# Performance work log

Measured on AMD Instinct MI355X. Metric: run time of the kernel, lower is better.

The kernel has to match this reference:

```python
import jax, jax.numpy as jnp
import numpy as np

P = 32
EPS = 1e-5

def setup_inputs() -> dict:
    key = jax.random.key(0)
    ks = jax.random.split(key, 6)
    B, C, H, W = 2, 256, 512, 512
    h_past = jax.random.normal(ks[0], (B, C, H, W), dtype=jnp.float32)
    scale = jnp.ones((C,), jnp.float32)
    shift = jnp.zeros((C,), jnp.float32)
    # depthwise 3x3: torch Conv2d(ch, ch, 3, groups=ch) weight shape (C,1,3,3)
    dw_w = jax.random.normal(ks[1], (C, 1, 3, 3), dtype=jnp.float32) * (1.0 / 3.0)
    dw_b = jax.random.normal(ks[2], (C,), dtype=jnp.float32) * 0.02
    # pointwise 1x1: weight (C_out, C_in)
    pw_w = jax.random.normal(ks[3], (C, C), dtype=jnp.float32) * (1.0 / np.sqrt(C))
    pw_b = jax.random.normal(ks[4], (C,), dtype=jnp.float32) * 0.02
    return {"h_past": h_past, "scale": scale, "shift": shift,
            "dw_w": dw_w, "dw_b": dw_b, "pw_w": pw_w, "pw_b": pw_b}

def reference(h_past, scale, shift, dw_w, dw_b, pw_w, pw_b):
    B, C, H, W = h_past.shape
    NRp, NCp = H // P, W // P
    # block-mean pool: [B,C,NRp,P,NCp,P] -> [B,C,NRp,NCp]
    x = h_past.reshape(B, C, NRp, P, NCp, P).mean(axis=(3, 5))
    # channel norm (mean/var over channel dim, unbiased=False)
    mu = x.mean(axis=1, keepdims=True)
    var = x.var(axis=1, keepdims=True)
    x = (x - mu) * jax.lax.rsqrt(var + EPS)
    x = x * scale[None, :, None, None] + shift[None, :, None, None]
    # depthwise 3x3 conv, padding=1
    x = jax.lax.conv_general_dilated(
        x, dw_w, window_strides=(1, 1), padding=((1, 1), (1, 1)),
        feature_group_count=C,
        dimension_numbers=("NCHW", "OIHW", "NCHW"))
    x = x + dw_b[None, :, None, None]
    # exact GELU (torch F.gelu default)
    x = jax.nn.gelu(x, approximate=False)
    # pointwise 1x1 conv
    x = jnp.einsum("bchw,oc->bohw", x, pw_w) + pw_b[None, :, None, None]
    # broadcast-upsample back to full H x W
    x_full = jnp.broadcast_to(x[:, :, :, None, :, None], (B, C, NRp, P, NCp, P))
    return x_full.reshape(B, C, NRp * P, NCp * P)
```

## Files before the change

kernel.cpp:

```cpp
#include <hip/hip_runtime.h>
#include <math.h>

constexpr int B = 2, C = 256, H = 512, W = 512, P = 32;
constexpr int NR = H / P;
constexpr int NC = W / P;
constexpr int NPOS = NR * NC;
constexpr float EPS = 1e-5f;

typedef float floatx4 __attribute__((ext_vector_type(4)));

__global__ void pool_kernel(const float* __restrict__ h_past,
                            float* __restrict__ xp) {
    int bid = blockIdx.x;
    int br = bid & 15;
    int c  = (bid >> 4) & 255;
    int b  = bid >> 12;
    const floatx4* src =
        (const floatx4*)(h_past + (((size_t)(b * C + c)) * H + (size_t)br * P) * W);
    int t    = threadIdx.x;
    int f4   = t & 127;
    int row0 = t >> 7;
    float s = 0.f;
#pragma unroll
    for (int k = 0; k < 16; ++k) {
        floatx4 v = src[(row0 + 2 * k) * 128 + f4];
        s += v.x + v.y + v.z + v.w;
    }
    __shared__ float part[256];
    part[t] = s;
    __syncthreads();
    if (t < 16) {
        float acc = 0.f;
#pragma unroll
        for (int j = 0; j < 8; ++j)
            acc += part[t * 8 + j] + part[128 + t * 8 + j];
        xp[((size_t)(b * NPOS + br * NC + t)) * C + c] = acc * (1.0f / (P * P));
    }
}

__global__ void stats_kernel(const float* __restrict__ xp,
                             float* __restrict__ mu_arr,
                             float* __restrict__ rs_arr) {
    int bid = blockIdx.x;
    int t = threadIdx.x;
    float v = xp[(size_t)bid * C + t];
    __shared__ float red[8];
    float s = v;
#pragma unroll
    for (int off = 32; off > 0; off >>= 1) s += __shfl_down(s, off, 64);
    int wave = t >> 6, lane = t & 63;
    if (lane == 0) red[wave] = s;
    __syncthreads();
    float mu = (red[0] + red[1] + red[2] + red[3]) * (1.0f / C);
    float d = v - mu;
    float s2 = d * d;
#pragma unroll
    for (int off = 32; off > 0; off >>= 1) s2 += __shfl_down(s2, off, 64);
    if (lane == 0) red[4 + wave] = s2;
    __syncthreads();
    if (t == 0) {
        float var = (red[4] + red[5] + red[6] + red[7]) * (1.0f / C);
        mu_arr[bid] = mu;
        rs_arr[bid] = rsqrtf(var + EPS);
    }
}

__global__ void pwt_kernel(const float* __restrict__ pw_w,
                           floatx4* __restrict__ pw_t) {
    int idx = blockIdx.x * 256 + threadIdx.x;
    int c4 = idx >> 8;
    int o  = idx & 255;
    const float* src = pw_w + o * C + 4 * c4;
    floatx4 v = {src[0], src[1], src[2], src[3]};
    pw_t[idx] = v;
}

__device__ inline float gelu_exact(float x) {
    return 0.5f * x * (1.0f + erff(x * 0.70710678118654752440f));
}

__global__ void fused_kernel(const float* __restrict__ xp,
                             const float* __restrict__ mu_arr,
                             const float* __restrict__ rs_arr,
                             const float* __restrict__ scale,
                             const float* __restrict__ shift,
                             const float* __restrict__ dw_w,
                             const float* __restrict__ dw_b,
                             const floatx4* __restrict__ pw_t,
                             const float* __restrict__ pw_b,
                             float* __restrict__ z) {
    int bid = blockIdx.x;
    int p = bid & 255;
    int b = bid >> 8;
    int h = p >> 4;
    int w = p & 15;
    int c = threadIdx.x;

    float sc = scale[c];
    float sh = shift[c];
    const float* wt  = dw_w + c * 9;
    const float* xpb = xp + (size_t)b * NPOS * C;
    const float* mub = mu_arr + b * NPOS;
    const float* rsb = rs_arr + b * NPOS;

    float acc = 0.f;
#pragma unroll
    for (int kh = 0; kh < 3; ++kh) {
        int hh = h + kh - 1;
        if (hh < 0 || hh >= NR) continue;
#pragma unroll
        for (int kw = 0; kw < 3; ++kw) {
            int ww = w + kw - 1;
            if (ww < 0 || ww >= NC) continue;
            int q = hh * NC + ww;
            float xv = xpb[(size_t)q * C + c];
            float xn = (xv - mub[q]) * rsb[q] * sc + sh;
            acc += xn * wt[kh * 3 + kw];
        }
    }
    float yv = gelu_exact(acc + dw_b[c]);

    __shared__ float ys[256];
    ys[c] = yv;
    __syncthreads();

    const floatx4* yv4 = (const floatx4*)ys;
    float acc2 = 0.f;
#pragma unroll 4
    for (int c4 = 0; c4 < 64; ++c4) {
        floatx4 wv = pw_t[c4 * 256 + c];
        floatx4 vv = yv4[c4];
        acc2 += wv.x * vv.x + wv.y * vv.y + wv.z * vv.z + wv.w * vv.w;
    }
    z[(size_t)bid * C + c] = acc2 + pw_b[c];
}

__global__ void up_kernel(const float* __restrict__ z,
                          floatx4* __restrict__ out) {
    const int total = B * C * H * (W / 4);
    for (int idx = blockIdx.x * 256 + threadIdx.x; idx < total;
         idx += gridDim.x * 256) {
        int w4 = idx & 127;
        int h  = (idx >> 7) & 511;
        int bc = idx >> 16;
        int b  = bc >> 8;
        int c  = bc & 255;
        int p  = (h >> 5) * NC + (w4 >> 3);
        float v = z[((size_t)(b * NPOS + p)) * C + c];
        floatx4 o = {v, v, v, v};
        out[idx] = o;
    }
}

extern "C" void kernel_launch(void* const* d_in, const int* in_sizes, int n_in,
                              void* d_out, int out_size, void* d_ws, size_t ws_size,
                              hipStream_t stream) {
    const float* h_past = (const float*)d_in[0];
    const float* scale  = (const float*)d_in[1];
    const float* shift  = (const float*)d_in[2];
    const float* dw_w   = (const float*)d_in[3];
    const float* dw_b   = (const float*)d_in[4];
    const float* pw_w   = (const float*)d_in[5];
    const float* pw_b   = (const float*)d_in[6];
    float* out = (float*)d_out;

    float* ws = (float*)d_ws;
    const int SMALL = B * C * NPOS;
    float* xp   = ws;
    float* z    = ws + SMALL;
    float* mu   = ws + 2 * SMALL;
    float* rs   = mu + B * NPOS;
    floatx4* pw_t = (floatx4*)(rs + B * NPOS);

    pwt_kernel<<<64, 256, 0, stream>>>(pw_w, pw_t);
    pool_kernel<<<B * C * NR, 256, 0, stream>>>(h_past, xp);
    stats_kernel<<<B * NPOS, 256, 0, stream>>>(xp, mu, rs);
    fused_kernel<<<B * NPOS, 256, 0, stream>>>(xp, mu, rs, scale, shift,
                                               dw_w, dw_b, pw_t, pw_b, z);
    up_kernel<<<32768, 256, 0, stream>>>(z, (floatx4*)out);
}
```

Before: 895.7 us.

## Merge all stages into one cooperative kernel with grid-wide syncs

```diff
diff --git a/kernel.cpp b/kernel.cpp
--- a/kernel.cpp
+++ b/kernel.cpp
@@ -1,5 +1,8 @@
 #include <hip/hip_runtime.h>
+#include <hip/hip_cooperative_groups.h>
 #include <math.h>
+
+namespace cg = cooperative_groups;
 
 constexpr int B = 2, C = 256, H = 512, W = 512, P = 32;
 constexpr int NR = H / P;
@@ -7,148 +10,148 @@
 constexpr int NPOS = NR * NC;
 constexpr float EPS = 1e-5f;
 
+constexpr int GRID = 1024;
+
 typedef float floatx4 __attribute__((ext_vector_type(4)));
-
-__global__ void pool_kernel(const float* __restrict__ h_past,
-                            float* __restrict__ xp) {
-    int bid = blockIdx.x;
-    int br = bid & 15;
-    int c  = (bid >> 4) & 255;
-    int b  = bid >> 12;
-    const floatx4* src =
-        (const floatx4*)(h_past + (((size_t)(b * C + c)) * H + (size_t)br * P) * W);
-    int t    = threadIdx.x;
-    int f4   = t & 127;
-    int row0 = t >> 7;
-    float s = 0.f;
-#pragma unroll
-    for (int k = 0; k < 16; ++k) {
-        floatx4 v = src[(row0 + 2 * k) * 128 + f4];
-        s += v.x + v.y + v.z + v.w;
-    }
-    __shared__ float part[256];
-    part[t] = s;
-    __syncthreads();
-    if (t < 16) {
-        float acc = 0.f;
-#pragma unroll
-        for (int j = 0; j < 8; ++j)
-            acc += part[t * 8 + j] + part[128 + t * 8 + j];
-        xp[((size_t)(b * NPOS + br * NC + t)) * C + c] = acc * (1.0f / (P * P));
-    }
-}
-
-__global__ void stats_kernel(const float* __restrict__ xp,
-                             float* __restrict__ mu_arr,
-                             float* __restrict__ rs_arr) {
-    int bid = blockIdx.x;
-    int t = threadIdx.x;
-    float v = xp[(size_t)bid * C + t];
-    __shared__ float red[8];
-    float s = v;
-#pragma unroll
-    for (int off = 32; off > 0; off >>= 1) s += __shfl_down(s, off, 64);
-    int wave = t >> 6, lane = t & 63;
-    if (lane == 0) red[wave] = s;
-    __syncthreads();
-    float mu = (red[0] + red[1] + red[2] + red[3]) * (1.0f / C);
-    float d = v - mu;
-    float s2 = d * d;
-#pragma unroll
-    for (int off = 32; off > 0; off >>= 1) s2 += __shfl_down(s2, off, 64);
-    if (lane == 0) red[4 + wave] = s2;
-    __syncthreads();
-    if (t == 0) {
-        float var = (red[4] + red[5] + red[6] + red[7]) * (1.0f / C);
-        mu_arr[bid] = mu;
-        rs_arr[bid] = rsqrtf(var + EPS);
-    }
-}
-
-__global__ void pwt_kernel(const float* __restrict__ pw_w,
-                           floatx4* __restrict__ pw_t) {
-    int idx = blockIdx.x * 256 + threadIdx.x;
-    int c4 = idx >> 8;
-    int o  = idx & 255;
-    const float* src = pw_w + o * C + 4 * c4;
-    floatx4 v = {src[0], src[1], src[2], src[3]};
-    pw_t[idx] = v;
-}
 
 __device__ inline float gelu_exact(float x) {
     return 0.5f * x * (1.0f + erff(x * 0.70710678118654752440f));
 }
 
-__global__ void fused_kernel(const float* __restrict__ xp,
-                             const float* __restrict__ mu_arr,
-                             const float* __restrict__ rs_arr,
-                             const float* __restrict__ scale,
-                             const float* __restrict__ shift,
-                             const float* __restrict__ dw_w,
-                             const float* __restrict__ dw_b,
-                             const floatx4* __restrict__ pw_t,
-                             const float* __restrict__ pw_b,
-                             float* __restrict__ z) {
-    int bid = blockIdx.x;
-    int p = bid & 255;
-    int b = bid >> 8;
-    int h = p >> 4;
-    int w = p & 15;
-    int c = threadIdx.x;
+__global__ __launch_bounds__(256, 4) void mega_kernel(
+    const float* __restrict__ h_past,
+    const float* __restrict__ scale, const float* __restrict__ shift,
+    const float* __restrict__ dw_w, const float* __restrict__ dw_b,
+    const float* __restrict__ pw_w, const float* __restrict__ pw_b,
+    float* __restrict__ xp, float* __restrict__ z,
+    float* __restrict__ mu_arr, float* __restrict__ rs_arr,
+    floatx4* __restrict__ pw_t,
+    floatx4* __restrict__ out)
+{
+    cg::grid_group grid = cg::this_grid();
+    const int t = threadIdx.x;
+    const int bid = blockIdx.x;
+    __shared__ float sm[256];
+    __shared__ float red[8];
 
-    float sc = scale[c];
-    float sh = shift[c];
-    const float* wt  = dw_w + c * 9;
-    const float* xpb = xp + (size_t)b * NPOS * C;
-    const float* mub = mu_arr + b * NPOS;
-    const float* rsb = rs_arr + b * NPOS;
-
-    float acc = 0.f;
+    {
+        int f4 = t & 127;
+        int row0 = t >> 7;
+        for (int i = 0; i < 8; ++i) {
+            int s = bid * 8 + i;
+            int br = s & 15;
+            int c  = (s >> 4) & 255;
+            int b  = s >> 12;
+            const floatx4* src = (const floatx4*)(
+                h_past + (((size_t)(b * C + c)) * H + (size_t)br * P) * W);
+            float acc = 0.f;
 #pragma unroll
-    for (int kh = 0; kh < 3; ++kh) {
-        int hh = h + kh - 1;
-        if (hh < 0 || hh >= NR) continue;
+            for (int k = 0; k < 16; ++k) {
+                floatx4 v = src[(row0 + 2 * k) * 128 + f4];
+                acc += v.x + v.y + v.z + v.w;
+            }
+            sm[t] = acc;
+            __syncthreads();
+            if (t < 16) {
+                float a2 = 0.f;
 #pragma unroll
-        for (int kw = 0; kw < 3; ++kw) {
-            int ww = w + kw - 1;
-            if (ww < 0 || ww >= NC) continue;
-            int q = hh * NC + ww;
-            float xv = xpb[(size_t)q * C + c];
-            float xn = (xv - mub[q]) * rsb[q] * sc + sh;
-            acc += xn * wt[kh * 3 + kw];
+                for (int j = 0; j < 8; ++j)
+                    a2 += sm[t * 8 + j] + sm[128 + t * 8 + j];
+                xp[((size_t)(b * NPOS + br * NC + t)) * C + c] = a2 * (1.0f / (P * P));
+            }
+            __syncthreads();
         }
     }
-    float yv = gelu_exact(acc + dw_b[c]);
+    __threadfence();
+    grid.sync();
 
-    __shared__ float ys[256];
-    ys[c] = yv;
-    __syncthreads();
+    if (bid < B * NPOS) {
+        float v = xp[(size_t)bid * C + t];
+        float s = v;
+#pragma unroll
+        for (int off = 32; off > 0; off >>= 1) s += __shfl_down(s, off, 64);
+        int wave = t >> 6, lane = t & 63;
+        if (lane == 0) red[wave] = s;
+        __syncthreads();
+        float mu = (red[0] + red[1] + red[2] + red[3]) * (1.0f / C);
+        float d = v - mu;
+        float s2 = d * d;
+#pragma unroll
+        for (int off = 32; off > 0; off >>= 1) s2 += __shfl_down(s2, off, 64);
+        if (lane == 0) red[4 + wave] = s2;
+        __syncthreads();
+        if (t == 0) {
+            float var = (red[4] + red[5] + red[6] + red[7]) * (1.0f / C);
+            mu_arr[bid] = mu;
+            rs_arr[bid] = rsqrtf(var + EPS);
+        }
+    } else if (bid < B * NPOS + 64) {
+        int idx = (bid - B * NPOS) * 256 + t;
+        int c4 = idx >> 8;
+        int o  = idx & 255;
+        const float* srcw = pw_w + o * C + 4 * c4;
+        floatx4 v = {srcw[0], srcw[1], srcw[2], srcw[3]};
+        pw_t[idx] = v;
+    }
+    __threadfence();
+    grid.sync();
 
-    const floatx4* yv4 = (const floatx4*)ys;
-    float acc2 = 0.f;
+    if (bid < B * NPOS) {
+        int p = bid & 255;
+        int b = bid >> 8;
+        int h = p >> 4;
+        int w = p & 15;
+        int c = t;
+        float sc = scale[c];
+        float sh = shift[c];
+        const float* wt  = dw_w + c * 9;
+        const float* xpb = xp + (size_t)b * NPOS * C;
+        const float* mub = mu_arr + b * NPOS;
+        const float* rsb = rs_arr + b * NPOS;
+        float acc = 0.f;
+#pragma unroll
+        for (int kh = 0; kh < 3; ++kh) {
+            int hh = h + kh - 1;
+            if (hh < 0 || hh >= NR) continue;
+#pragma unroll
+            for (int kw = 0; kw < 3; ++kw) {
+                int ww = w + kw - 1;
+                if (ww < 0 || ww >= NC) continue;
+                int q = hh * NC + ww;
+                float xv = xpb[(size_t)q * C + c];
+                float xn = (xv - mub[q]) * rsb[q] * sc + sh;
+                acc += xn * wt[kh * 3 + kw];
+            }
+        }
+        float yv = gelu_exact(acc + dw_b[c]);
+        sm[c] = yv;
+        __syncthreads();
+        const floatx4* yv4 = (const floatx4*)sm;
+        float acc2 = 0.f;
 #pragma unroll 4
-    for (int c4 = 0; c4 < 64; ++c4) {
-        floatx4 wv = pw_t[c4 * 256 + c];
-        floatx4 vv = yv4[c4];
-        acc2 += wv.x * vv.x + wv.y * vv.y + wv.z * vv.z + wv.w * vv.w;
+        for (int c4 = 0; c4 < 64; ++c4) {
+            floatx4 wv = pw_t[c4 * 256 + c];
+            floatx4 vv = yv4[c4];
+            acc2 += wv.x * vv.x + wv.y * vv.y + wv.z * vv.z + wv.w * vv.w;
+        }
+        z[(size_t)bid * C + c] = acc2 + pw_b[c];
     }
-    z[(size_t)bid * C + c] = acc2 + pw_b[c];
-}
+    __threadfence();
+    grid.sync();
 
-__global__ void up_kernel(const float* __restrict__ z,
-                          floatx4* __restrict__ out) {
-    const int total = B * C * H * (W / 4);
-    for (int idx = blockIdx.x * 256 + threadIdx.x; idx < total;
-         idx += gridDim.x * 256) {
-        int w4 = idx & 127;
-        int h  = (idx >> 7) & 511;
-        int bc = idx >> 16;
-        int b  = bc >> 8;
-        int c  = bc & 255;
-        int p  = (h >> 5) * NC + (w4 >> 3);
-        float v = z[((size_t)(b * NPOS + p)) * C + c];
-        floatx4 o = {v, v, v, v};
-        out[idx] = o;
+    {
+        const int total = B * C * H * (W / 4);
+        for (int idx = bid * 256 + t; idx < total; idx += GRID * 256) {
+            int w4 = idx & 127;
+            int h  = (idx >> 7) & 511;
+            int bc = idx >> 16;
+            int b  = bc >> 8;
+            int c  = bc & 255;
+            int p  = (h >> 5) * NC + (w4 >> 3);
+            float v = z[((size_t)(b * NPOS + p)) * C + c];
+            floatx4 o = {v, v, v, v};
+            out[idx] = o;
+        }
     }
 }
 
@@ -166,16 +169,19 @@
 
     float* ws = (float*)d_ws;
     const int SMALL = B * C * NPOS;
-    float* xp   = ws;
-    float* z    = ws + SMALL;
-    float* mu   = ws + 2 * SMALL;
-    float* rs   = mu + B * NPOS;
+    float* xp = ws;
+    float* z  = ws + SMALL;
+    float* mu = ws + 2 * SMALL;
+    float* rs = mu + B * NPOS;
     floatx4* pw_t = (floatx4*)(rs + B * NPOS);
+    floatx4* outv = (floatx4*)out;
 
-    pwt_kernel<<<64, 256, 0, stream>>>(pw_w, pw_t);
-    pool_kernel<<<B * C * NR, 256, 0, stream>>>(h_past, xp);
-    stats_kernel<<<B * NPOS, 256, 0, stream>>>(xp, mu, rs);
-    fused_kernel<<<B * NPOS, 256, 0, stream>>>(xp, mu, rs, scale, shift,
-                                               dw_w, dw_b, pw_t, pw_b, z);
-    up_kernel<<<32768, 256, 0, stream>>>(z, (floatx4*)out);
+    void* args[] = {
+        (void*)&h_past, (void*)&scale, (void*)&shift,
+        (void*)&dw_w, (void*)&dw_b, (void*)&pw_w, (void*)&pw_b,
+        (void*)&xp, (void*)&z, (void*)&mu, (void*)&rs,
+        (void*)&pw_t, (void*)&outv,
+    };
+    hipLaunchCooperativeKernel((const void*)mega_kernel, dim3(GRID), dim3(256),
+                               args, 0, stream);
 }
```

New measurement: 1.509 ms. +68.4%, slower.
